# Kernel optimization log

Measured on AMD Instinct MI355X. Metric: run time of the kernel, lower is better.

The kernel has to match this reference:

```python
import jax, jax.numpy as jnp
import numpy as np

B, T, C, HS = 8, 2048, 1024, 64


def setup_inputs() -> dict:
    key = jax.random.key(0)
    kx, kq, kk, kv = jax.random.split(key, 4)
    x = jax.random.normal(kx, (B, T, C), dtype=jnp.float32)
    # torch Linear(C, HS, bias=False): weight [HS, C], y = x @ W.T -> store as [C, HS]
    Wq = jax.random.normal(kq, (C, HS), dtype=jnp.float32) * (C ** -0.5)
    Wk = jax.random.normal(kk, (C, HS), dtype=jnp.float32) * (C ** -0.5)
    Wv = jax.random.normal(kv, (C, HS), dtype=jnp.float32) * (C ** -0.5)
    return {"x": x, "Wq": Wq, "Wk": Wk, "Wv": Wv}


def reference(x, Wq, Wk, Wv):
    _, t, c = x.shape
    q = jnp.einsum('btc,ch->bth', x, Wq)
    k = jnp.einsum('btc,ch->bth', x, Wk)
    v = jnp.einsum('btc,ch->bth', x, Wv)
    # NOTE: original scales by C**-0.5 (hidden_dim), not head_size**-0.5
    scores = jnp.einsum('bth,bsh->bts', q, k) * (c ** -0.5)  # [B,T,T]
    causal = jnp.tril(jnp.ones((t, t), dtype=bool))
    scores = jnp.where(causal, scores, -jnp.inf)
    probs = jax.nn.softmax(scores, axis=-1)  # dropout p=0.0 -> identity
    out = jnp.einsum('bts,bsh->bth', probs, v)  # [B,T,HS]
    return out
```

## Files before the change

kernel.cpp:

```cpp
#include <hip/hip_runtime.h>
#include <hip/hip_bf16.h>

#define B_ 8
#define T_ 2048
#define C_ 1024
#define HS_ 64

typedef float f32x4 __attribute__((ext_vector_type(4)));
typedef __bf16 bf16x8 __attribute__((ext_vector_type(8)));
typedef __bf16 bf16x4 __attribute__((ext_vector_type(4)));

__device__ __forceinline__ void gld_lds16(const void* g, void* l) {
    __builtin_amdgcn_global_load_lds(
        (const __attribute__((address_space(1))) void*)g,
        (__attribute__((address_space(3))) void*)l, 16, 0, 0);
}


__global__ __launch_bounds__(256) void wt_kernel(const float* __restrict__ Wq,
                                                 const float* __restrict__ Wk,
                                                 const float* __restrict__ Wv,
                                                 __bf16* __restrict__ wt) {
    __shared__ float tile[64][65];
    int mb = blockIdx.x >> 4;
    int k0 = (blockIdx.x & 15) * 64;
    const float* W = (mb == 0) ? Wq : (mb == 1 ? Wk : Wv);
    int c = threadIdx.x & 63;
#pragma unroll
    for (int r = threadIdx.x >> 6; r < 64; r += 4)
        tile[r][c] = W[(size_t)(k0 + r) * 64 + c];
    __syncthreads();
    float scale = (mb == 0) ? 0.03125f : 1.0f;
#pragma unroll
    for (int i = 0; i < 2; ++i) {
        int u = threadIdx.x + i * 256;
        int n  = u >> 3;
        int ch = u & 7;
        int src = (ch ^ (n & 7)) * 8;
        bf16x8 v;
#pragma unroll
        for (int e = 0; e < 8; ++e)
            v[e] = (__bf16)(tile[src + e][n] * scale);
        *(bf16x8*)(wt + (size_t)(mb * 64 + n) * C_ + k0 + ch * 8) = v;
    }
}

__global__ __launch_bounds__(512) void qkv_kernel(const float* __restrict__ x,
                                                  const __bf16* __restrict__ wt,
                                                  __bf16* __restrict__ qf,
                                                  __bf16* __restrict__ kf,
                                                  __bf16* __restrict__ vf) {
    __shared__ __align__(16) char smem[57344];
    __bf16* xs0 = (__bf16*)smem;
    __bf16* xs1 = (__bf16*)(smem + 4096);
    __bf16* ws0 = (__bf16*)(smem + 8192);
    __bf16* ws1 = (__bf16*)(smem + 32768);

    const int tid = threadIdx.x;
    const int w = tid >> 6, lane = tid & 63, lq = lane & 15, lg = lane >> 4;
    const int m0 = blockIdx.x * 32;
    const int mt = w & 1;
    const int ntb = (w >> 1) * 3;

    f32x4 acc[3];
#pragma unroll
    for (int i = 0; i < 3; ++i) acc[i] = (f32x4)0.0f;

    const int xrow = tid >> 3, xch = tid & 7;
    float4 xr0, xr1;
    const int wslot0 = w * 3 * 64 + lane;

    if (tid < 256) {
        const float* xp = x + (size_t)(m0 + xrow) * C_ + xch * 8;
        xr0 = *(const float4*)xp;
        xr1 = *(const float4*)(xp + 4);
    }
#pragma unroll
    for (int s = 0; s < 3; ++s) {
        int slot = wslot0 + s * 64;
        gld_lds16(wt + (size_t)(slot >> 3) * C_ + (slot & 7) * 8,
                  ws0 + (w * 3 + s) * 512);
    }
    if (tid < 256) {
        bf16x8 xb;
#pragma unroll
        for (int j = 0; j < 4; ++j) { xb[j] = (__bf16)xr0[j]; xb[4 + j] = (__bf16)xr1[j]; }
        *(bf16x8*)(xs0 + xrow * 64 + ((xch ^ (xrow & 7)) * 8)) = xb;
    }

    for (int kt = 0; kt < 16; ++kt) {
        __syncthreads();
        __bf16* xsc = (kt & 1) ? xs1 : xs0;
        __bf16* wsc = (kt & 1) ? ws1 : ws0;
        __bf16* xsn = (kt & 1) ? xs0 : xs1;
        __bf16* wsn = (kt & 1) ? ws0 : ws1;
        if (kt < 15) {
            int k0 = (kt + 1) * 64;
            if (tid < 256) {
                const float* xp = x + (size_t)(m0 + xrow) * C_ + k0 + xch * 8;
                xr0 = *(const float4*)xp;
                xr1 = *(const float4*)(xp + 4);
            }
#pragma unroll
            for (int s = 0; s < 3; ++s) {
                int slot = wslot0 + s * 64;
                gld_lds16(wt + (size_t)(slot >> 3) * C_ + k0 + (slot & 7) * 8,
                          wsn + (w * 3 + s) * 512);
            }
        }
#pragma unroll
        for (int ks = 0; ks < 2; ++ks) {
            int r = mt * 16 + lq;
            bf16x8 a = *(const bf16x8*)(xsc + r * 64 + (((ks * 4 + lg) ^ (r & 7)) * 8));
#pragma unroll
            for (int i = 0; i < 3; ++i) {
                int rw = (ntb + i) * 16 + lq;
                bf16x8 b = *(const bf16x8*)(wsc + rw * 64 + (((ks * 4 + lg) ^ (rw & 7)) * 8));
                acc[i] = __builtin_amdgcn_mfma_f32_16x16x32_bf16(a, b, acc[i], 0, 0, 0);
            }
        }
        if (kt < 15 && tid < 256) {
            bf16x8 xb;
#pragma unroll
            for (int j = 0; j < 4; ++j) { xb[j] = (__bf16)xr0[j]; xb[4 + j] = (__bf16)xr1[j]; }
            *(bf16x8*)(xsn + xrow * 64 + ((xch ^ (xrow & 7)) * 8)) = xb;
        }
    }
    __syncthreads();

    __bf16(*obuf)[208] = (__bf16(*)[208])smem;
#pragma unroll
    for (int i = 0; i < 3; ++i)
#pragma unroll
        for (int r = 0; r < 4; ++r)
            obuf[mt * 16 + lg * 4 + r][(ntb + i) * 16 + lq] = (__bf16)acc[i][r];
    __syncthreads();

    if (w < 4) {
        int mg = w & 1, half = w >> 1;
        size_t qt16 = (size_t)(m0 >> 4) + mg;
        bf16x8 vq = *(const bf16x8*)&obuf[mg * 16 + lq][half * 32 + lg * 8];
        bf16x8 vk = *(const bf16x8*)&obuf[mg * 16 + lq][64 + half * 32 + lg * 8];
        *(bf16x8*)(qf + ((qt16 * 2 + half) * 64 + lane) * 8) = vq;
        *(bf16x8*)(kf + ((qt16 * 2 + half) * 64 + lane) * 8) = vk;
    } else {
        int ntv = w - 4;
        bf16x8 vv;
#pragma unroll
        for (int j = 0; j < 8; ++j)
            vv[j] = obuf[lg * 8 + j][128 + ntv * 16 + lq];
        size_t kt32 = (size_t)(m0 >> 5);
        *(bf16x8*)(vf + ((kt32 * 4 + ntv) * 64 + lane) * 8) = vv;
    }
}

__global__ __launch_bounds__(512, 4) void attn_kernel(const __bf16* __restrict__ qf,
                                                      const __bf16* __restrict__ kf,
                                                      const __bf16* __restrict__ vf,
                                                      float* __restrict__ out) {
    __shared__ float olds[8][16][64];
    __shared__ float mlds[8][16], llds[8][16];
    __shared__ __align__(16) __bf16 plds[8][16 * 72];

    int w    = threadIdx.x >> 6;
    int lane = threadIdx.x & 63;
    int lq = lane & 15, lg = lane >> 4;

    int b  = blockIdx.x & 7;
    int q0 = (63 - (blockIdx.x >> 3)) * 32;
    int qs = w >> 2;
    int wk = w & 3;
    int qt = q0 + qs * 16;

    size_t qbase = ((size_t)b * 128 + (qt >> 4)) * 2;
    bf16x8 aq0 = *(const bf16x8*)(qf + ((qbase + 0) * 64 + lane) * 8);
    bf16x8 aq1 = *(const bf16x8*)(qf + ((qbase + 1) * 64 + lane) * 8);

    f32x4 o[4];
#pragma unroll
    for (int nt = 0; nt < 4; ++nt) o[nt] = (f32x4)0.0f;
    float m_s = -1e30f, l_s = 0.f;

    __bf16* pw = &plds[w][0];

    int ntiles = (qt + 79) >> 6;
    for (int kt = wk; kt < ntiles; kt += 4) {
        int s0 = kt * 64;
        f32x4 s[4];
        __builtin_amdgcn_s_setprio(1);
#pragma unroll
        for (int ct = 0; ct < 4; ++ct) {
            size_t kbase = ((size_t)b * 128 + (s0 >> 4) + ct) * 2;
            bf16x8 k0 = *(const bf16x8*)(kf + ((kbase + 0) * 64 + lane) * 8);
            bf16x8 k1 = *(const bf16x8*)(kf + ((kbase + 1) * 64 + lane) * 8);
            f32x4 a = (f32x4)0.0f;
            a = __builtin_amdgcn_mfma_f32_16x16x32_bf16(k0, aq0, a, 0, 0, 0);
            a = __builtin_amdgcn_mfma_f32_16x16x32_bf16(k1, aq1, a, 0, 0, 0);
            s[ct] = a;
        }
        __builtin_amdgcn_s_setprio(0);
        if (s0 + 63 > qt) {
#pragma unroll
            for (int ct = 0; ct < 4; ++ct)
#pragma unroll
                for (int r = 0; r < 4; ++r)
                    if (s0 + ct * 16 + lg * 4 + r > qt + lq) s[ct][r] = -1e30f;
        }
        bf16x8 bv[2][4];
#pragma unroll
        for (int ks = 0; ks < 2; ++ks)
#pragma unroll
            for (int nt = 0; nt < 4; ++nt)
                bv[ks][nt] = *(const bf16x8*)(vf +
                    (((size_t)(b * 64 + (s0 >> 5) + ks) * 4 + nt) * 64 + lane) * 8);
        float pm = -1e30f;
#pragma unroll
        for (int ct = 0; ct < 4; ++ct)
#pragma unroll
            for (int r = 0; r < 4; ++r) pm = fmaxf(pm, s[ct][r]);
        pm = fmaxf(pm, __shfl_xor(pm, 16));
        pm = fmaxf(pm, __shfl_xor(pm, 32));
        bool need = __any(pm > m_s);
        float al = 1.0f;
        if (need) {
            float mn = fmaxf(m_s, pm);
            al = __expf(m_s - mn);
            m_s = mn;
        }
        float rs = 0.f;
        f32x4 p[4];
#pragma unroll
        for (int ct = 0; ct < 4; ++ct)
#pragma unroll
            for (int r = 0; r < 4; ++r) {
                p[ct][r] = __expf(s[ct][r] - m_s);
                rs += p[ct][r];
            }
        rs += __shfl_xor(rs, 16);
        rs += __shfl_xor(rs, 32);
        if (need) {
            l_s = l_s * al + rs;
            float alr[4];
#pragma unroll
            for (int r = 0; r < 4; ++r) alr[r] = __shfl(al, lg * 4 + r);
#pragma unroll
            for (int nt = 0; nt < 4; ++nt)
#pragma unroll
                for (int r = 0; r < 4; ++r) o[nt][r] *= alr[r];
        } else {
            l_s += rs;
        }
#pragma unroll
        for (int ct = 0; ct < 4; ++ct) {
            bf16x4 qv;
#pragma unroll
            for (int r = 0; r < 4; ++r) qv[r] = (__bf16)p[ct][r];
            *(bf16x4*)&pw[lq * 72 + ct * 16 + lg * 4] = qv;
        }
        asm volatile("" ::: "memory");
        bf16x8 pa0 = *(const bf16x8*)&pw[lq * 72 + lg * 8];
        bf16x8 pa1 = *(const bf16x8*)&pw[lq * 72 + 32 + lg * 8];
        __builtin_amdgcn_s_setprio(1);
#pragma unroll
        for (int nt = 0; nt < 4; ++nt) {
            o[nt] = __builtin_amdgcn_mfma_f32_16x16x32_bf16(pa0, bv[0][nt], o[nt], 0, 0, 0);
            o[nt] = __builtin_amdgcn_mfma_f32_16x16x32_bf16(pa1, bv[1][nt], o[nt], 0, 0, 0);
        }
        __builtin_amdgcn_s_setprio(0);
    }

    asm volatile("" ::: "memory");
#pragma unroll
    for (int nt = 0; nt < 4; ++nt)
#pragma unroll
        for (int r = 0; r < 4; ++r)
            olds[w][lg * 4 + r][nt * 16 + lq] = o[nt][r];
    if (lg == 0) {
        mlds[w][lq] = m_s;
        llds[w][lq] = l_s;
    }
    __syncthreads();

    int row = threadIdx.x >> 4;
    int c4  = (threadIdx.x & 15) * 4;
    int wb  = (row >> 4) * 4;
    int r16 = row & 15;
    float M = -1e30f;
#pragma unroll
    for (int w2 = 0; w2 < 4; ++w2) M = fmaxf(M, mlds[wb + w2][r16]);
    float L = 0.f;
    f32x4 oa = (f32x4)0.0f;
#pragma unroll
    for (int w2 = 0; w2 < 4; ++w2) {
        float sc = __expf(mlds[wb + w2][r16] - M);
        L += sc * llds[wb + w2][r16];
        const float* op = &olds[wb + w2][r16][c4];
#pragma unroll
        for (int j = 0; j < 4; ++j) oa[j] += sc * op[j];
    }
    float inv = 1.0f / L;
    float4 st;
    st.x = oa[0] * inv; st.y = oa[1] * inv; st.z = oa[2] * inv; st.w = oa[3] * inv;
    *(float4*)(out + ((size_t)b * T_ + q0 + row) * HS_ + c4) = st;
}

extern "C" void kernel_launch(void* const* d_in, const int* in_sizes, int n_in,
                              void* d_out, int out_size, void* d_ws, size_t ws_size,
                              hipStream_t stream) {
    const float* x  = (const float*)d_in[0];
    const float* Wq = (const float*)d_in[1];
    const float* Wk = (const float*)d_in[2];
    const float* Wv = (const float*)d_in[3];
    char* ws = (char*)d_ws;
    __bf16* wt = (__bf16*)ws;
    __bf16* qf = (__bf16*)(ws + 393216);
    __bf16* kf = (__bf16*)(ws + 2490368);
    __bf16* vf = (__bf16*)(ws + 4587520);
    float* out = (float*)d_out;

    wt_kernel<<<dim3(48), dim3(256), 0, stream>>>(Wq, Wk, Wv, wt);
    qkv_kernel<<<dim3(512), dim3(512), 0, stream>>>(x, wt, qf, kf, vf);
    attn_kernel<<<dim3(512), dim3(512), 0, stream>>>(qf, kf, vf, out);
}
```

Before: 39.01 us.

## Switch attention to 32x32x16 MFMA with 32-key tiles split across 8 waves

Reworks the attention kernel to use 32x32x16 bf16 MFMA instead of 16x16x32. Each of the 8 waves now handles all 32 queries of the block over a strided subset of 32-key tiles, instead of two groups of 4 waves each handling 16 queries over 64-key tiles. The QKV projection kernel writes Q/K/V in a new fragment layout matching the larger MFMA operands. Wave partials are stored to LDS in bf16 and merged across 8 waves, which cuts per-tile overhead and LDS footprint but lowers the precision of the partial outputs and makes the final merge longer.

```diff
diff --git a/kernel.cpp b/kernel.cpp
--- a/kernel.cpp
+++ b/kernel.cpp
@@ -7,6 +7,7 @@
 #define HS_ 64
 
 typedef float f32x4 __attribute__((ext_vector_type(4)));
+typedef float f32x16 __attribute__((ext_vector_type(16)));
 typedef __bf16 bf16x8 __attribute__((ext_vector_type(8)));
 typedef __bf16 bf16x4 __attribute__((ext_vector_type(4)));
 
@@ -58,6 +59,7 @@
 
     const int tid = threadIdx.x;
     const int w = tid >> 6, lane = tid & 63, lq = lane & 15, lg = lane >> 4;
+    const int l31 = lane & 31, lh = lane >> 5;
     const int m0 = blockIdx.x * 32;
     const int mt = w & 1;
     const int ntb = (w >> 1) * 3;
@@ -136,21 +138,20 @@
             obuf[mt * 16 + lg * 4 + r][(ntb + i) * 16 + lq] = (__bf16)acc[i][r];
     __syncthreads();
 
+    size_t t32g = (size_t)blockIdx.x;
     if (w < 4) {
-        int mg = w & 1, half = w >> 1;
-        size_t qt16 = (size_t)(m0 >> 4) + mg;
-        bf16x8 vq = *(const bf16x8*)&obuf[mg * 16 + lq][half * 32 + lg * 8];
-        bf16x8 vk = *(const bf16x8*)&obuf[mg * 16 + lq][64 + half * 32 + lg * 8];
-        *(bf16x8*)(qf + ((qt16 * 2 + half) * 64 + lane) * 8) = vq;
-        *(bf16x8*)(kf + ((qt16 * 2 + half) * 64 + lane) * 8) = vk;
+        int ks = w;
+        bf16x8 vq = *(const bf16x8*)&obuf[l31][ks * 16 + lh * 8];
+        bf16x8 vk = *(const bf16x8*)&obuf[l31][64 + ks * 16 + lh * 8];
+        *(bf16x8*)(qf + ((t32g * 4 + ks) * 64 + lane) * 8) = vq;
+        *(bf16x8*)(kf + ((t32g * 4 + ks) * 64 + lane) * 8) = vk;
     } else {
-        int ntv = w - 4;
+        int dt = (w - 4) >> 1, ksl = (w - 4) & 1;
         bf16x8 vv;
 #pragma unroll
         for (int j = 0; j < 8; ++j)
-            vv[j] = obuf[lg * 8 + j][128 + ntv * 16 + lq];
-        size_t kt32 = (size_t)(m0 >> 5);
-        *(bf16x8*)(vf + ((kt32 * 4 + ntv) * 64 + lane) * 8) = vv;
+            vv[j] = obuf[ksl * 16 + lh * 8 + j][128 + dt * 32 + l31];
+        *(bf16x8*)(vf + (((t32g * 2 + dt) * 2 + ksl) * 64 + lane) * 8) = vv;
     }
 }
 
@@ -158,67 +159,59 @@
                                                       const __bf16* __restrict__ kf,
                                                       const __bf16* __restrict__ vf,
                                                       float* __restrict__ out) {
-    __shared__ float olds[8][16][64];
-    __shared__ float mlds[8][16], llds[8][16];
-    __shared__ __align__(16) __bf16 plds[8][16 * 72];
-
-    int w    = threadIdx.x >> 6;
-    int lane = threadIdx.x & 63;
-    int lq = lane & 15, lg = lane >> 4;
-
-    int b  = blockIdx.x & 7;
-    int q0 = (63 - (blockIdx.x >> 3)) * 32;
-    int qs = w >> 2;
-    int wk = w & 3;
-    int qt = q0 + qs * 16;
-
-    size_t qbase = ((size_t)b * 128 + (qt >> 4)) * 2;
-    bf16x8 aq0 = *(const bf16x8*)(qf + ((qbase + 0) * 64 + lane) * 8);
-    bf16x8 aq1 = *(const bf16x8*)(qf + ((qbase + 1) * 64 + lane) * 8);
-
-    f32x4 o[4];
-#pragma unroll
-    for (int nt = 0; nt < 4; ++nt) o[nt] = (f32x4)0.0f;
+    __shared__ __align__(16) char smem[34816];
+    float* mlds = (float*)(smem + 32768);
+    float* llds = (float*)(smem + 33792);
+
+    const int tid = threadIdx.x;
+    const int w = tid >> 6, lane = tid & 63;
+    const int l31 = lane & 31, lh = lane >> 5;
+
+    const int b  = blockIdx.x & 7;
+    const int q0 = (63 - (blockIdx.x >> 3)) * 32;
+
+    size_t qt32g = (size_t)b * 64 + (q0 >> 5);
+    bf16x8 bq[4];
+#pragma unroll
+    for (int ks = 0; ks < 4; ++ks)
+        bq[ks] = *(const bf16x8*)(qf + ((qt32g * 4 + ks) * 64 + lane) * 8);
+
+    f32x16 o2[2];
+    o2[0] = (f32x16)0.0f;
+    o2[1] = (f32x16)0.0f;
     float m_s = -1e30f, l_s = 0.f;
 
-    __bf16* pw = &plds[w][0];
-
-    int ntiles = (qt + 79) >> 6;
-    for (int kt = wk; kt < ntiles; kt += 4) {
-        int s0 = kt * 64;
-        f32x4 s[4];
+    __bf16* pP = (__bf16*)(smem + w * 2304);
+
+    int ntiles = (q0 >> 5) + 1;
+    for (int kt = w; kt < ntiles; kt += 8) {
+        int s0 = kt * 32;
+        size_t kt32g = (size_t)b * 64 + (s0 >> 5);
+        f32x16 st = (f32x16)0.0f;
         __builtin_amdgcn_s_setprio(1);
 #pragma unroll
-        for (int ct = 0; ct < 4; ++ct) {
-            size_t kbase = ((size_t)b * 128 + (s0 >> 4) + ct) * 2;
-            bf16x8 k0 = *(const bf16x8*)(kf + ((kbase + 0) * 64 + lane) * 8);
-            bf16x8 k1 = *(const bf16x8*)(kf + ((kbase + 1) * 64 + lane) * 8);
-            f32x4 a = (f32x4)0.0f;
-            a = __builtin_amdgcn_mfma_f32_16x16x32_bf16(k0, aq0, a, 0, 0, 0);
-            a = __builtin_amdgcn_mfma_f32_16x16x32_bf16(k1, aq1, a, 0, 0, 0);
-            s[ct] = a;
+        for (int ks = 0; ks < 4; ++ks) {
+            bf16x8 ka = *(const bf16x8*)(kf + ((kt32g * 4 + ks) * 64 + lane) * 8);
+            st = __builtin_amdgcn_mfma_f32_32x32x16_bf16(ka, bq[ks], st, 0, 0, 0);
         }
         __builtin_amdgcn_s_setprio(0);
-        if (s0 + 63 > qt) {
-#pragma unroll
-            for (int ct = 0; ct < 4; ++ct)
+        if (s0 + 31 > q0) {
+#pragma unroll
+            for (int g = 0; g < 4; ++g)
 #pragma unroll
                 for (int r = 0; r < 4; ++r)
-                    if (s0 + ct * 16 + lg * 4 + r > qt + lq) s[ct][r] = -1e30f;
-        }
-        bf16x8 bv[2][4];
-#pragma unroll
-        for (int ks = 0; ks < 2; ++ks)
-#pragma unroll
-            for (int nt = 0; nt < 4; ++nt)
-                bv[ks][nt] = *(const bf16x8*)(vf +
-                    (((size_t)(b * 64 + (s0 >> 5) + ks) * 4 + nt) * 64 + lane) * 8);
+                    if (s0 + g * 8 + 4 * lh + r > q0 + l31) st[g * 4 + r] = -1e30f;
+        }
+        bf16x8 bv[2][2];
+#pragma unroll
+        for (int dt = 0; dt < 2; ++dt)
+#pragma unroll
+            for (int ksl = 0; ksl < 2; ++ksl)
+                bv[dt][ksl] = *(const bf16x8*)(vf +
+                    (((kt32g * 2 + dt) * 2 + ksl) * 64 + lane) * 8);
         float pm = -1e30f;
 #pragma unroll
-        for (int ct = 0; ct < 4; ++ct)
-#pragma unroll
-            for (int r = 0; r < 4; ++r) pm = fmaxf(pm, s[ct][r]);
-        pm = fmaxf(pm, __shfl_xor(pm, 16));
+        for (int e = 0; e < 16; ++e) pm = fmaxf(pm, st[e]);
         pm = fmaxf(pm, __shfl_xor(pm, 32));
         bool need = __any(pm > m_s);
         float al = 1.0f;
@@ -228,80 +221,81 @@
             m_s = mn;
         }
         float rs = 0.f;
-        f32x4 p[4];
-#pragma unroll
-        for (int ct = 0; ct < 4; ++ct)
-#pragma unroll
-            for (int r = 0; r < 4; ++r) {
-                p[ct][r] = __expf(s[ct][r] - m_s);
-                rs += p[ct][r];
-            }
-        rs += __shfl_xor(rs, 16);
+#pragma unroll
+        for (int e = 0; e < 16; ++e) {
+            st[e] = __expf(st[e] - m_s);
+            rs += st[e];
+        }
         rs += __shfl_xor(rs, 32);
         if (need) {
             l_s = l_s * al + rs;
-            float alr[4];
-#pragma unroll
-            for (int r = 0; r < 4; ++r) alr[r] = __shfl(al, lg * 4 + r);
-#pragma unroll
-            for (int nt = 0; nt < 4; ++nt)
-#pragma unroll
-                for (int r = 0; r < 4; ++r) o[nt][r] *= alr[r];
+#pragma unroll
+            for (int g = 0; g < 4; ++g)
+#pragma unroll
+                for (int r = 0; r < 4; ++r) {
+                    float alr = __shfl(al, g * 8 + 4 * lh + r);
+                    o2[0][g * 4 + r] *= alr;
+                    o2[1][g * 4 + r] *= alr;
+                }
         } else {
             l_s += rs;
         }
 #pragma unroll
-        for (int ct = 0; ct < 4; ++ct) {
-            bf16x4 qv;
-#pragma unroll
-            for (int r = 0; r < 4; ++r) qv[r] = (__bf16)p[ct][r];
-            *(bf16x4*)&pw[lq * 72 + ct * 16 + lg * 4] = qv;
+        for (int g = 0; g < 4; ++g) {
+            bf16x4 pk;
+#pragma unroll
+            for (int r = 0; r < 4; ++r) pk[r] = (__bf16)st[g * 4 + r];
+            *(bf16x4*)&pP[l31 * 36 + g * 8 + 4 * lh] = pk;
         }
         asm volatile("" ::: "memory");
-        bf16x8 pa0 = *(const bf16x8*)&pw[lq * 72 + lg * 8];
-        bf16x8 pa1 = *(const bf16x8*)&pw[lq * 72 + 32 + lg * 8];
+        bf16x8 pa0 = *(const bf16x8*)&pP[l31 * 36 + lh * 8];
+        bf16x8 pa1 = *(const bf16x8*)&pP[l31 * 36 + 16 + lh * 8];
         __builtin_amdgcn_s_setprio(1);
 #pragma unroll
-        for (int nt = 0; nt < 4; ++nt) {
-            o[nt] = __builtin_amdgcn_mfma_f32_16x16x32_bf16(pa0, bv[0][nt], o[nt], 0, 0, 0);
-            o[nt] = __builtin_amdgcn_mfma_f32_16x16x32_bf16(pa1, bv[1][nt], o[nt], 0, 0, 0);
+        for (int dt = 0; dt < 2; ++dt) {
+            o2[dt] = __builtin_amdgcn_mfma_f32_32x32x16_bf16(pa0, bv[dt][0], o2[dt], 0, 0, 0);
+            o2[dt] = __builtin_amdgcn_mfma_f32_32x32x16_bf16(pa1, bv[dt][1], o2[dt], 0, 0, 0);
         }
         __builtin_amdgcn_s_setprio(0);
     }
 
-    asm volatile("" ::: "memory");
-#pragma unroll
-    for (int nt = 0; nt < 4; ++nt)
-#pragma unroll
-        for (int r = 0; r < 4; ++r)
-            olds[w][lg * 4 + r][nt * 16 + lq] = o[nt][r];
-    if (lg == 0) {
-        mlds[w][lq] = m_s;
-        llds[w][lq] = l_s;
-    }
-    __syncthreads();
-
-    int row = threadIdx.x >> 4;
-    int c4  = (threadIdx.x & 15) * 4;
-    int wb  = (row >> 4) * 4;
-    int r16 = row & 15;
+    __syncthreads();
+    __bf16* olds_w = (__bf16*)(smem + w * 4096);
+#pragma unroll
+    for (int dt = 0; dt < 2; ++dt)
+#pragma unroll
+        for (int g = 0; g < 4; ++g) {
+            bf16x4 pk;
+#pragma unroll
+            for (int r = 0; r < 4; ++r) pk[r] = (__bf16)o2[dt][g * 4 + r];
+            *(bf16x4*)&olds_w[(l31 + dt * 32) * 32 + g * 8 + 4 * lh] = pk;
+        }
+    if (lh == 0) {
+        mlds[w * 32 + l31] = m_s;
+        llds[w * 32 + l31] = l_s;
+    }
+    __syncthreads();
+
+    int q  = tid >> 4;
+    int c4 = (tid & 15) * 4;
     float M = -1e30f;
 #pragma unroll
-    for (int w2 = 0; w2 < 4; ++w2) M = fmaxf(M, mlds[wb + w2][r16]);
+    for (int w2 = 0; w2 < 8; ++w2) M = fmaxf(M, mlds[w2 * 32 + q]);
     float L = 0.f;
     f32x4 oa = (f32x4)0.0f;
 #pragma unroll
-    for (int w2 = 0; w2 < 4; ++w2) {
-        float sc = __expf(mlds[wb + w2][r16] - M);
-        L += sc * llds[wb + w2][r16];
-        const float* op = &olds[wb + w2][r16][c4];
-#pragma unroll
-        for (int j = 0; j < 4; ++j) oa[j] += sc * op[j];
+    for (int w2 = 0; w2 < 8; ++w2) {
+        float sc = __expf(mlds[w2 * 32 + q] - M);
+        L += sc * llds[w2 * 32 + q];
+        const __bf16* op = (const __bf16*)(smem + w2 * 4096);
+#pragma unroll
+        for (int k = 0; k < 4; ++k)
+            oa[k] += sc * (float)op[(c4 + k) * 32 + q];
     }
     float inv = 1.0f / L;
-    float4 st;
-    st.x = oa[0] * inv; st.y = oa[1] * inv; st.z = oa[2] * inv; st.w = oa[3] * inv;
-    *(float4*)(out + ((size_t)b * T_ + q0 + row) * HS_ + c4) = st;
+    float4 stv;
+    stv.x = oa[0] * inv; stv.y = oa[1] * inv; stv.z = oa[2] * inv; stv.w = oa[3] * inv;
+    *(float4*)(out + ((size_t)b * T_ + q0 + q) * HS_ + c4) = stv;
 }
 
 extern "C" void kernel_launch(void* const* d_in, const int* in_sizes, int n_in,
```

Result: slower. 47.58 us (+22.0%).

## Fuse weight transpose, QKV projection and attention into one persistent kernel with grid barriers

Applied to the files above, without the earlier changes.

Merges the three kernel launches into a single kernel and separates the phases with atomic-counter grid-wide barriers, with a memset resetting the counter before launch. The goal is to remove two kernel launch gaps and the tail drain between dependent stages. In exchange every block must wait at each barrier, so the kernel relies on all 512 blocks being co-resident, and the memset adds a small extra operation. Shared memory is reused across phases, and the fused kernel uses launch bounds of (512, 4) for all phases.

```diff
diff --git a/kernel.cpp b/kernel.cpp
--- a/kernel.cpp
+++ b/kernel.cpp
@@ -16,292 +16,306 @@
         (__attribute__((address_space(3))) void*)l, 16, 0, 0);
 }
 
-
-__global__ __launch_bounds__(256) void wt_kernel(const float* __restrict__ Wq,
-                                                 const float* __restrict__ Wk,
-                                                 const float* __restrict__ Wv,
-                                                 __bf16* __restrict__ wt) {
-    __shared__ float tile[64][65];
-    int mb = blockIdx.x >> 4;
-    int k0 = (blockIdx.x & 15) * 64;
-    const float* W = (mb == 0) ? Wq : (mb == 1 ? Wk : Wv);
-    int c = threadIdx.x & 63;
-#pragma unroll
-    for (int r = threadIdx.x >> 6; r < 64; r += 4)
-        tile[r][c] = W[(size_t)(k0 + r) * 64 + c];
+__device__ __forceinline__ void gbar(unsigned* cnt, unsigned target) {
     __syncthreads();
-    float scale = (mb == 0) ? 0.03125f : 1.0f;
-#pragma unroll
-    for (int i = 0; i < 2; ++i) {
-        int u = threadIdx.x + i * 256;
-        int n  = u >> 3;
-        int ch = u & 7;
-        int src = (ch ^ (n & 7)) * 8;
-        bf16x8 v;
-#pragma unroll
-        for (int e = 0; e < 8; ++e)
-            v[e] = (__bf16)(tile[src + e][n] * scale);
-        *(bf16x8*)(wt + (size_t)(mb * 64 + n) * C_ + k0 + ch * 8) = v;
-    }
-}
-
-__global__ __launch_bounds__(512) void qkv_kernel(const float* __restrict__ x,
-                                                  const __bf16* __restrict__ wt,
-                                                  __bf16* __restrict__ qf,
-                                                  __bf16* __restrict__ kf,
-                                                  __bf16* __restrict__ vf) {
-    __shared__ __align__(16) char smem[57344];
-    __bf16* xs0 = (__bf16*)smem;
-    __bf16* xs1 = (__bf16*)(smem + 4096);
-    __bf16* ws0 = (__bf16*)(smem + 8192);
-    __bf16* ws1 = (__bf16*)(smem + 32768);
-
-    const int tid = threadIdx.x;
-    const int w = tid >> 6, lane = tid & 63, lq = lane & 15, lg = lane >> 4;
-    const int m0 = blockIdx.x * 32;
-    const int mt = w & 1;
-    const int ntb = (w >> 1) * 3;
-
-    f32x4 acc[3];
-#pragma unroll
-    for (int i = 0; i < 3; ++i) acc[i] = (f32x4)0.0f;
-
-    const int xrow = tid >> 3, xch = tid & 7;
-    float4 xr0, xr1;
-    const int wslot0 = w * 3 * 64 + lane;
-
-    if (tid < 256) {
-        const float* xp = x + (size_t)(m0 + xrow) * C_ + xch * 8;
-        xr0 = *(const float4*)xp;
-        xr1 = *(const float4*)(xp + 4);
-    }
-#pragma unroll
-    for (int s = 0; s < 3; ++s) {
-        int slot = wslot0 + s * 64;
-        gld_lds16(wt + (size_t)(slot >> 3) * C_ + (slot & 7) * 8,
-                  ws0 + (w * 3 + s) * 512);
-    }
-    if (tid < 256) {
-        bf16x8 xb;
-#pragma unroll
-        for (int j = 0; j < 4; ++j) { xb[j] = (__bf16)xr0[j]; xb[4 + j] = (__bf16)xr1[j]; }
-        *(bf16x8*)(xs0 + xrow * 64 + ((xch ^ (xrow & 7)) * 8)) = xb;
-    }
-
-    for (int kt = 0; kt < 16; ++kt) {
-        __syncthreads();
-        __bf16* xsc = (kt & 1) ? xs1 : xs0;
-        __bf16* wsc = (kt & 1) ? ws1 : ws0;
-        __bf16* xsn = (kt & 1) ? xs0 : xs1;
-        __bf16* wsn = (kt & 1) ? ws0 : ws1;
-        if (kt < 15) {
-            int k0 = (kt + 1) * 64;
-            if (tid < 256) {
-                const float* xp = x + (size_t)(m0 + xrow) * C_ + k0 + xch * 8;
-                xr0 = *(const float4*)xp;
-                xr1 = *(const float4*)(xp + 4);
-            }
-#pragma unroll
-            for (int s = 0; s < 3; ++s) {
-                int slot = wslot0 + s * 64;
-                gld_lds16(wt + (size_t)(slot >> 3) * C_ + k0 + (slot & 7) * 8,
-                          wsn + (w * 3 + s) * 512);
-            }
-        }
-#pragma unroll
-        for (int ks = 0; ks < 2; ++ks) {
-            int r = mt * 16 + lq;
-            bf16x8 a = *(const bf16x8*)(xsc + r * 64 + (((ks * 4 + lg) ^ (r & 7)) * 8));
-#pragma unroll
-            for (int i = 0; i < 3; ++i) {
-                int rw = (ntb + i) * 16 + lq;
-                bf16x8 b = *(const bf16x8*)(wsc + rw * 64 + (((ks * 4 + lg) ^ (rw & 7)) * 8));
-                acc[i] = __builtin_amdgcn_mfma_f32_16x16x32_bf16(a, b, acc[i], 0, 0, 0);
-            }
-        }
-        if (kt < 15 && tid < 256) {
-            bf16x8 xb;
-#pragma unroll
-            for (int j = 0; j < 4; ++j) { xb[j] = (__bf16)xr0[j]; xb[4 + j] = (__bf16)xr1[j]; }
-            *(bf16x8*)(xsn + xrow * 64 + ((xch ^ (xrow & 7)) * 8)) = xb;
-        }
+    if (threadIdx.x == 0) {
+        __threadfence();
+        atomicAdd(cnt, 1u);
+        while (atomicAdd(cnt, 0u) < target)
+            __builtin_amdgcn_s_sleep(2);
+        __threadfence();
     }
     __syncthreads();
-
-    __bf16(*obuf)[208] = (__bf16(*)[208])smem;
-#pragma unroll
-    for (int i = 0; i < 3; ++i)
-#pragma unroll
-        for (int r = 0; r < 4; ++r)
-            obuf[mt * 16 + lg * 4 + r][(ntb + i) * 16 + lq] = (__bf16)acc[i][r];
-    __syncthreads();
-
-    if (w < 4) {
-        int mg = w & 1, half = w >> 1;
-        size_t qt16 = (size_t)(m0 >> 4) + mg;
-        bf16x8 vq = *(const bf16x8*)&obuf[mg * 16 + lq][half * 32 + lg * 8];
-        bf16x8 vk = *(const bf16x8*)&obuf[mg * 16 + lq][64 + half * 32 + lg * 8];
-        *(bf16x8*)(qf + ((qt16 * 2 + half) * 64 + lane) * 8) = vq;
-        *(bf16x8*)(kf + ((qt16 * 2 + half) * 64 + lane) * 8) = vk;
-    } else {
-        int ntv = w - 4;
-        bf16x8 vv;
-#pragma unroll
-        for (int j = 0; j < 8; ++j)
-            vv[j] = obuf[lg * 8 + j][128 + ntv * 16 + lq];
-        size_t kt32 = (size_t)(m0 >> 5);
-        *(bf16x8*)(vf + ((kt32 * 4 + ntv) * 64 + lane) * 8) = vv;
+}
+
+
+__global__ __launch_bounds__(512, 4) void fused_kernel(
+        const float* __restrict__ x,
+        const float* __restrict__ Wq,
+        const float* __restrict__ Wk,
+        const float* __restrict__ Wv,
+        __bf16* __restrict__ wt,
+        __bf16* __restrict__ qf,
+        __bf16* __restrict__ kf,
+        __bf16* __restrict__ vf,
+        float* __restrict__ out,
+        unsigned* __restrict__ cnt) {
+    __shared__ __align__(16) char smem[57344];
+    const int tid = threadIdx.x;
+
+    if (blockIdx.x < 48) {
+        float(*tile)[65] = (float(*)[65])smem;
+        int mb = blockIdx.x >> 4;
+        int k0 = (blockIdx.x & 15) * 64;
+        const float* W = (mb == 0) ? Wq : (mb == 1 ? Wk : Wv);
+        int c = tid & 63;
+#pragma unroll
+        for (int r = tid >> 6; r < 64; r += 8)
+            tile[r][c] = W[(size_t)(k0 + r) * 64 + c];
+        __syncthreads();
+        float scale = (mb == 0) ? 0.03125f : 1.0f;
+        {
+            int n  = tid >> 3;
+            int ch = tid & 7;
+            int src = (ch ^ (n & 7)) * 8;
+            bf16x8 v;
+#pragma unroll
+            for (int e = 0; e < 8; ++e)
+                v[e] = (__bf16)(tile[src + e][n] * scale);
+            *(bf16x8*)(wt + (size_t)(mb * 64 + n) * C_ + k0 + ch * 8) = v;
+        }
     }
-}
-
-__global__ __launch_bounds__(512, 4) void attn_kernel(const __bf16* __restrict__ qf,
-                                                      const __bf16* __restrict__ kf,
-                                                      const __bf16* __restrict__ vf,
-                                                      float* __restrict__ out) {
-    __shared__ float olds[8][16][64];
-    __shared__ float mlds[8][16], llds[8][16];
-    __shared__ __align__(16) __bf16 plds[8][16 * 72];
-
-    int w    = threadIdx.x >> 6;
-    int lane = threadIdx.x & 63;
-    int lq = lane & 15, lg = lane >> 4;
-
-    int b  = blockIdx.x & 7;
-    int q0 = (63 - (blockIdx.x >> 3)) * 32;
-    int qs = w >> 2;
-    int wk = w & 3;
-    int qt = q0 + qs * 16;
-
-    size_t qbase = ((size_t)b * 128 + (qt >> 4)) * 2;
-    bf16x8 aq0 = *(const bf16x8*)(qf + ((qbase + 0) * 64 + lane) * 8);
-    bf16x8 aq1 = *(const bf16x8*)(qf + ((qbase + 1) * 64 + lane) * 8);
-
-    f32x4 o[4];
-#pragma unroll
-    for (int nt = 0; nt < 4; ++nt) o[nt] = (f32x4)0.0f;
-    float m_s = -1e30f, l_s = 0.f;
-
-    __bf16* pw = &plds[w][0];
-
-    int ntiles = (qt + 79) >> 6;
-    for (int kt = wk; kt < ntiles; kt += 4) {
-        int s0 = kt * 64;
-        f32x4 s[4];
-        __builtin_amdgcn_s_setprio(1);
-#pragma unroll
-        for (int ct = 0; ct < 4; ++ct) {
-            size_t kbase = ((size_t)b * 128 + (s0 >> 4) + ct) * 2;
-            bf16x8 k0 = *(const bf16x8*)(kf + ((kbase + 0) * 64 + lane) * 8);
-            bf16x8 k1 = *(const bf16x8*)(kf + ((kbase + 1) * 64 + lane) * 8);
-            f32x4 a = (f32x4)0.0f;
-            a = __builtin_amdgcn_mfma_f32_16x16x32_bf16(k0, aq0, a, 0, 0, 0);
-            a = __builtin_amdgcn_mfma_f32_16x16x32_bf16(k1, aq1, a, 0, 0, 0);
-            s[ct] = a;
-        }
-        __builtin_amdgcn_s_setprio(0);
-        if (s0 + 63 > qt) {
+    gbar(cnt, 512);
+
+    {
+        __bf16* xs0 = (__bf16*)smem;
+        __bf16* xs1 = (__bf16*)(smem + 4096);
+        __bf16* ws0 = (__bf16*)(smem + 8192);
+        __bf16* ws1 = (__bf16*)(smem + 32768);
+
+        const int w = tid >> 6, lane = tid & 63, lq = lane & 15, lg = lane >> 4;
+        const int m0 = blockIdx.x * 32;
+        const int mt = w & 1;
+        const int ntb = (w >> 1) * 3;
+
+        f32x4 acc[3];
+#pragma unroll
+        for (int i = 0; i < 3; ++i) acc[i] = (f32x4)0.0f;
+
+        const int xrow = tid >> 3, xch = tid & 7;
+        float4 xr0, xr1;
+        const int wslot0 = w * 3 * 64 + lane;
+
+        if (tid < 256) {
+            const float* xp = x + (size_t)(m0 + xrow) * C_ + xch * 8;
+            xr0 = *(const float4*)xp;
+            xr1 = *(const float4*)(xp + 4);
+        }
+#pragma unroll
+        for (int s = 0; s < 3; ++s) {
+            int slot = wslot0 + s * 64;
+            gld_lds16(wt + (size_t)(slot >> 3) * C_ + (slot & 7) * 8,
+                      ws0 + (w * 3 + s) * 512);
+        }
+        if (tid < 256) {
+            bf16x8 xb;
+#pragma unroll
+            for (int j = 0; j < 4; ++j) { xb[j] = (__bf16)xr0[j]; xb[4 + j] = (__bf16)xr1[j]; }
+            *(bf16x8*)(xs0 + xrow * 64 + ((xch ^ (xrow & 7)) * 8)) = xb;
+        }
+
+        for (int kt = 0; kt < 16; ++kt) {
+            __syncthreads();
+            __bf16* xsc = (kt & 1) ? xs1 : xs0;
+            __bf16* wsc = (kt & 1) ? ws1 : ws0;
+            __bf16* xsn = (kt & 1) ? xs0 : xs1;
+            __bf16* wsn = (kt & 1) ? ws0 : ws1;
+            if (kt < 15) {
+                int k0 = (kt + 1) * 64;
+                if (tid < 256) {
+                    const float* xp = x + (size_t)(m0 + xrow) * C_ + k0 + xch * 8;
+                    xr0 = *(const float4*)xp;
+                    xr1 = *(const float4*)(xp + 4);
+                }
+#pragma unroll
+                for (int s = 0; s < 3; ++s) {
+                    int slot = wslot0 + s * 64;
+                    gld_lds16(wt + (size_t)(slot >> 3) * C_ + k0 + (slot & 7) * 8,
+                              wsn + (w * 3 + s) * 512);
+                }
+            }
+#pragma unroll
+            for (int ks = 0; ks < 2; ++ks) {
+                int r = mt * 16 + lq;
+                bf16x8 a = *(const bf16x8*)(xsc + r * 64 + (((ks * 4 + lg) ^ (r & 7)) * 8));
+#pragma unroll
+                for (int i = 0; i < 3; ++i) {
+                    int rw = (ntb + i) * 16 + lq;
+                    bf16x8 b = *(const bf16x8*)(wsc + rw * 64 + (((ks * 4 + lg) ^ (rw & 7)) * 8));
+                    acc[i] = __builtin_amdgcn_mfma_f32_16x16x32_bf16(a, b, acc[i], 0, 0, 0);
+                }
+            }
+            if (kt < 15 && tid < 256) {
+                bf16x8 xb;
+#pragma unroll
+                for (int j = 0; j < 4; ++j) { xb[j] = (__bf16)xr0[j]; xb[4 + j] = (__bf16)xr1[j]; }
+                *(bf16x8*)(xsn + xrow * 64 + ((xch ^ (xrow & 7)) * 8)) = xb;
+            }
+        }
+        __syncthreads();
+
+        __bf16(*obuf)[208] = (__bf16(*)[208])smem;
+#pragma unroll
+        for (int i = 0; i < 3; ++i)
+#pragma unroll
+            for (int r = 0; r < 4; ++r)
+                obuf[mt * 16 + lg * 4 + r][(ntb + i) * 16 + lq] = (__bf16)acc[i][r];
+        __syncthreads();
+
+        if (w < 4) {
+            int mg = w & 1, half = w >> 1;
+            size_t qt16 = (size_t)(m0 >> 4) + mg;
+            bf16x8 vq = *(const bf16x8*)&obuf[mg * 16 + lq][half * 32 + lg * 8];
+            bf16x8 vk = *(const bf16x8*)&obuf[mg * 16 + lq][64 + half * 32 + lg * 8];
+            *(bf16x8*)(qf + ((qt16 * 2 + half) * 64 + lane) * 8) = vq;
+            *(bf16x8*)(kf + ((qt16 * 2 + half) * 64 + lane) * 8) = vk;
+        } else {
+            int ntv = w - 4;
+            bf16x8 vv;
+#pragma unroll
+            for (int j = 0; j < 8; ++j)
+                vv[j] = obuf[lg * 8 + j][128 + ntv * 16 + lq];
+            size_t kt32 = (size_t)(m0 >> 5);
+            *(bf16x8*)(vf + ((kt32 * 4 + ntv) * 64 + lane) * 8) = vv;
+        }
+    }
+    gbar(cnt, 1024);
+
+    {
+        float(*olds)[16][64] = (float(*)[16][64])smem;
+        float* mlds = (float*)(smem + 32768);
+        float* llds = (float*)(smem + 33280);
+        __bf16* plds = (__bf16*)(smem + 33792);
+
+        const int w = tid >> 6, lane = tid & 63, lq = lane & 15, lg = lane >> 4;
+
+        int b  = blockIdx.x & 7;
+        int q0 = (63 - (blockIdx.x >> 3)) * 32;
+        int qs = w >> 2;
+        int wk = w & 3;
+        int qt = q0 + qs * 16;
+
+        size_t qbase = ((size_t)b * 128 + (qt >> 4)) * 2;
+        bf16x8 aq0 = *(const bf16x8*)(qf + ((qbase + 0) * 64 + lane) * 8);
+        bf16x8 aq1 = *(const bf16x8*)(qf + ((qbase + 1) * 64 + lane) * 8);
+
+        f32x4 o[4];
+#pragma unroll
+        for (int nt = 0; nt < 4; ++nt) o[nt] = (f32x4)0.0f;
+        float m_s = -1e30f, l_s = 0.f;
+
+        __bf16* pw = plds + w * (16 * 72);
+
+        int ntiles = (qt + 79) >> 6;
+        for (int kt = wk; kt < ntiles; kt += 4) {
+            int s0 = kt * 64;
+            f32x4 s[4];
+            __builtin_amdgcn_s_setprio(1);
+#pragma unroll
+            for (int ct = 0; ct < 4; ++ct) {
+                size_t kbase = ((size_t)b * 128 + (s0 >> 4) + ct) * 2;
+                bf16x8 k0 = *(const bf16x8*)(kf + ((kbase + 0) * 64 + lane) * 8);
+                bf16x8 k1 = *(const bf16x8*)(kf + ((kbase + 1) * 64 + lane) * 8);
+                f32x4 a = (f32x4)0.0f;
+                a = __builtin_amdgcn_mfma_f32_16x16x32_bf16(k0, aq0, a, 0, 0, 0);
+                a = __builtin_amdgcn_mfma_f32_16x16x32_bf16(k1, aq1, a, 0, 0, 0);
+                s[ct] = a;
+            }
+            __builtin_amdgcn_s_setprio(0);
+            if (s0 + 63 > qt) {
+#pragma unroll
+                for (int ct = 0; ct < 4; ++ct)
+#pragma unroll
+                    for (int r = 0; r < 4; ++r)
+                        if (s0 + ct * 16 + lg * 4 + r > qt + lq) s[ct][r] = -1e30f;
+            }
+            bf16x8 bv[2][4];
+#pragma unroll
+            for (int ks = 0; ks < 2; ++ks)
+#pragma unroll
+                for (int nt = 0; nt < 4; ++nt)
+                    bv[ks][nt] = *(const bf16x8*)(vf +
+                        (((size_t)(b * 64 + (s0 >> 5) + ks) * 4 + nt) * 64 + lane) * 8);
+            float pm = -1e30f;
 #pragma unroll
             for (int ct = 0; ct < 4; ++ct)
 #pragma unroll
-                for (int r = 0; r < 4; ++r)
-                    if (s0 + ct * 16 + lg * 4 + r > qt + lq) s[ct][r] = -1e30f;
-        }
-        bf16x8 bv[2][4];
-#pragma unroll
-        for (int ks = 0; ks < 2; ++ks)
-#pragma unroll
-            for (int nt = 0; nt < 4; ++nt)
-                bv[ks][nt] = *(const bf16x8*)(vf +
-                    (((size_t)(b * 64 + (s0 >> 5) + ks) * 4 + nt) * 64 + lane) * 8);
-        float pm = -1e30f;
-#pragma unroll
-        for (int ct = 0; ct < 4; ++ct)
-#pragma unroll
-            for (int r = 0; r < 4; ++r) pm = fmaxf(pm, s[ct][r]);
-        pm = fmaxf(pm, __shfl_xor(pm, 16));
-        pm = fmaxf(pm, __shfl_xor(pm, 32));
-        bool need = __any(pm > m_s);
-        float al = 1.0f;
-        if (need) {
-            float mn = fmaxf(m_s, pm);
-            al = __expf(m_s - mn);
-            m_s = mn;
-        }
-        float rs = 0.f;
-        f32x4 p[4];
-#pragma unroll
-        for (int ct = 0; ct < 4; ++ct)
-#pragma unroll
-            for (int r = 0; r < 4; ++r) {
-                p[ct][r] = __expf(s[ct][r] - m_s);
-                rs += p[ct][r];
-            }
-        rs += __shfl_xor(rs, 16);
-        rs += __shfl_xor(rs, 32);
-        if (need) {
-            l_s = l_s * al + rs;
-            float alr[4];
-#pragma unroll
-            for (int r = 0; r < 4; ++r) alr[r] = __shfl(al, lg * 4 + r);
-#pragma unroll
-            for (int nt = 0; nt < 4; ++nt)
-#pragma unroll
-                for (int r = 0; r < 4; ++r) o[nt][r] *= alr[r];
-        } else {
-            l_s += rs;
-        }
-#pragma unroll
-        for (int ct = 0; ct < 4; ++ct) {
-            bf16x4 qv;
-#pragma unroll
-            for (int r = 0; r < 4; ++r) qv[r] = (__bf16)p[ct][r];
-            *(bf16x4*)&pw[lq * 72 + ct * 16 + lg * 4] = qv;
-        }
-        asm volatile("" ::: "memory");
-        bf16x8 pa0 = *(const bf16x8*)&pw[lq * 72 + lg * 8];
-        bf16x8 pa1 = *(const bf16x8*)&pw[lq * 72 + 32 + lg * 8];
-        __builtin_amdgcn_s_setprio(1);
-#pragma unroll
-        for (int nt = 0; nt < 4; ++nt) {
-            o[nt] = __builtin_amdgcn_mfma_f32_16x16x32_bf16(pa0, bv[0][nt], o[nt], 0, 0, 0);
-            o[nt] = __builtin_amdgcn_mfma_f32_16x16x32_bf16(pa1, bv[1][nt], o[nt], 0, 0, 0);
-        }
-        __builtin_amdgcn_s_setprio(0);
+                for (int r = 0; r < 4; ++r) pm = fmaxf(pm, s[ct][r]);
+            pm = fmaxf(pm, __shfl_xor(pm, 16));
+            pm = fmaxf(pm, __shfl_xor(pm, 32));
+            bool need = __any(pm > m_s);
+            float al = 1.0f;
+            if (need) {
+                float mn = fmaxf(m_s, pm);
+                al = __expf(m_s - mn);
+                m_s = mn;
+            }
+            float rs = 0.f;
+            f32x4 p[4];
+#pragma unroll
+            for (int ct = 0; ct < 4; ++ct)
+#pragma unroll
+                for (int r = 0; r < 4; ++r) {
+                    p[ct][r] = __expf(s[ct][r] - m_s);
+                    rs += p[ct][r];
+                }
+            rs += __shfl_xor(rs, 16);
+            rs += __shfl_xor(rs, 32);
+            if (need) {
+                l_s = l_s * al + rs;
+                float alr[4];
+#pragma unroll
+                for (int r = 0; r < 4; ++r) alr[r] = __shfl(al, lg * 4 + r);
+#pragma unroll
+                for (int nt = 0; nt < 4; ++nt)
+#pragma unroll
+                    for (int r = 0; r < 4; ++r) o[nt][r] *= alr[r];
+            } else {
+                l_s += rs;
+            }
+#pragma unroll
+            for (int ct = 0; ct < 4; ++ct) {
+                bf16x4 qv;
+#pragma unroll
+                for (int r = 0; r < 4; ++r) qv[r] = (__bf16)p[ct][r];
+                *(bf16x4*)&pw[lq * 72 + ct * 16 + lg * 4] = qv;
+            }
+            asm volatile("" ::: "memory");
+            bf16x8 pa0 = *(const bf16x8*)&pw[lq * 72 + lg * 8];
+            bf16x8 pa1 = *(const bf16x8*)&pw[lq * 72 + 32 + lg * 8];
+            __builtin_amdgcn_s_setprio(1);
+#pragma unroll
+            for (int nt = 0; nt < 4; ++nt) {
+                o[nt] = __builtin_amdgcn_mfma_f32_16x16x32_bf16(pa0, bv[0][nt], o[nt], 0, 0, 0);
+                o[nt] = __builtin_amdgcn_mfma_f32_16x16x32_bf16(pa1, bv[1][nt], o[nt], 0, 0, 0);
+            }
+            __builtin_amdgcn_s_setprio(0);
+        }
+
+        __syncthreads();
+#pragma unroll
+        for (int nt = 0; nt < 4; ++nt)
+#pragma unroll
+            for (int r = 0; r < 4; ++r)
+                olds[w][lg * 4 + r][nt * 16 + lq] = o[nt][r];
+        if (lg == 0) {
+            mlds[w * 16 + lq] = m_s;
+            llds[w * 16 + lq] = l_s;
+        }
+        __syncthreads();
+
+        int row = tid >> 4;
+        int c4  = (tid & 15) * 4;
+        int wb  = (row >> 4) * 4;
+        int r16 = row & 15;
+        float M = -1e30f;
+#pragma unroll
+        for (int w2 = 0; w2 < 4; ++w2) M = fmaxf(M, mlds[(wb + w2) * 16 + r16]);
+        float L = 0.f;
+        f32x4 oa = (f32x4)0.0f;
+#pragma unroll
+        for (int w2 = 0; w2 < 4; ++w2) {
+            float sc = __expf(mlds[(wb + w2) * 16 + r16] - M);
+            L += sc * llds[(wb + w2) * 16 + r16];
+            const float* op = &olds[wb + w2][r16][c4];
+#pragma unroll
+            for (int j = 0; j < 4; ++j) oa[j] += sc * op[j];
+        }
+        float inv = 1.0f / L;
+        float4 st;
+        st.x = oa[0] * inv; st.y = oa[1] * inv; st.z = oa[2] * inv; st.w = oa[3] * inv;
+        *(float4*)(out + ((size_t)b * T_ + q0 + row) * HS_ + c4) = st;
     }
-
-    asm volatile("" ::: "memory");
-#pragma unroll
-    for (int nt = 0; nt < 4; ++nt)
-#pragma unroll
-        for (int r = 0; r < 4; ++r)
-            olds[w][lg * 4 + r][nt * 16 + lq] = o[nt][r];
-    if (lg == 0) {
-        mlds[w][lq] = m_s;
-        llds[w][lq] = l_s;
-    }
-    __syncthreads();
-
-    int row = threadIdx.x >> 4;
-    int c4  = (threadIdx.x & 15) * 4;
-    int wb  = (row >> 4) * 4;
-    int r16 = row & 15;
-    float M = -1e30f;
-#pragma unroll
-    for (int w2 = 0; w2 < 4; ++w2) M = fmaxf(M, mlds[wb + w2][r16]);
-    float L = 0.f;
-    f32x4 oa = (f32x4)0.0f;
-#pragma unroll
-    for (int w2 = 0; w2 < 4; ++w2) {
-        float sc = __expf(mlds[wb + w2][r16] - M);
-        L += sc * llds[wb + w2][r16];
-        const float* op = &olds[wb + w2][r16][c4];
-#pragma unroll
-        for (int j = 0; j < 4; ++j) oa[j] += sc * op[j];
-    }
-    float inv = 1.0f / L;
-    float4 st;
-    st.x = oa[0] * inv; st.y = oa[1] * inv; st.z = oa[2] * inv; st.w = oa[3] * inv;
-    *(float4*)(out + ((size_t)b * T_ + q0 + row) * HS_ + c4) = st;
 }
 
 extern "C" void kernel_launch(void* const* d_in, const int* in_sizes, int n_in,
@@ -316,9 +330,10 @@
     __bf16* qf = (__bf16*)(ws + 393216);
     __bf16* kf = (__bf16*)(ws + 2490368);
     __bf16* vf = (__bf16*)(ws + 4587520);
+    unsigned* cnt = (unsigned*)(ws + 6684672);
     float* out = (float*)d_out;
 
-    wt_kernel<<<dim3(48), dim3(256), 0, stream>>>(Wq, Wk, Wv, wt);
-    qkv_kernel<<<dim3(512), dim3(512), 0, stream>>>(x, wt, qf, kf, vf);
-    attn_kernel<<<dim3(512), dim3(512), 0, stream>>>(qf, kf, vf, out);
+    hipMemsetAsync(cnt, 0, 4, stream);
+    fused_kernel<<<dim3(512), dim3(512), 0, stream>>>(
+        x, Wq, Wk, Wv, wt, qf, kf, vf, out, cnt);
 }
```

New measurement: 125.6 us. 222% more time.
